# Optimization experiments

Measured on AMD Instinct MI355X. Metric: run time of the kernel, lower is better.

## Reference

```python
import jax, jax.numpy as jnp
import numpy as np

T, B, D = 256, 64, 512


def setup_inputs() -> dict:
    key = jax.random.key(0)
    ks = jax.random.split(key, 9)
    s = 1.0 / np.sqrt(D)  # torch Linear default init scale (uniform), use scaled normal
    return {
        "x": jax.random.normal(ks[0], (T, B, D), dtype=jnp.float32),
        "y": jax.random.normal(ks[1], (T, B, D), dtype=jnp.float32),
        "Wr": jax.random.normal(ks[2], (D, D), dtype=jnp.float32) * s,
        "Ur": jax.random.normal(ks[3], (D, D), dtype=jnp.float32) * s,
        "Wz": jax.random.normal(ks[4], (D, D), dtype=jnp.float32) * s,
        "Uz": jax.random.normal(ks[5], (D, D), dtype=jnp.float32) * s,
        "Wg": jax.random.normal(ks[6], (D, D), dtype=jnp.float32) * s,
        "Ug": jax.random.normal(ks[7], (D, D), dtype=jnp.float32) * s,
        "bg": jnp.full((D,), 2.0, dtype=jnp.float32),
    }


def reference(x, y, Wr, Ur, Wz, Uz, Wg, Ug, bg):
    # GTrXL gating unit. torch Linear(y) == y @ W.T
    r = jax.nn.sigmoid(jnp.einsum("tbd,ed->tbe", y, Wr) + jnp.einsum("tbd,ed->tbe", x, Ur))
    z = jax.nn.sigmoid(jnp.einsum("tbd,ed->tbe", y, Wz) + jnp.einsum("tbd,ed->tbe", x, Uz) - bg)
    h = jnp.tanh(jnp.einsum("tbd,ed->tbe", y, Wg) + jnp.einsum("tbd,ed->tbe", r * x, Ug))
    g = (1.0 - z) * x + z * h  # (T, B, D)
    return g
```

## Files before the change

### kernel.cpp

```cpp
#include <hip/hip_runtime.h>
#include <stdint.h>

typedef unsigned short u16;
typedef __attribute__((ext_vector_type(8))) __bf16 bf16x8;
typedef __attribute__((ext_vector_type(4))) float f32x4;

#define Dn 512
#define Mn 16384


__device__ __forceinline__ u16 f2bf(float f) {
  unsigned u = __float_as_uint(f);
  u += 0x7fffu + ((u >> 16) & 1u);
  return (u16)(u >> 16);
}

__device__ __forceinline__ float bf2f(u16 b) {
  return __uint_as_float(((unsigned)b) << 16);
}

__device__ __forceinline__ void async16(const u16* g, u16* l) {
  __builtin_amdgcn_global_load_lds(
      (const __attribute__((address_space(1))) unsigned int*)g,
      (__attribute__((address_space(3))) unsigned int*)l, 16, 0, 0);
}

__device__ __forceinline__ float sigmoidf_(float v) {
  return 1.f / (1.f + __expf(-v));
}

__global__ void cast_all(const float* __restrict__ y, const float* __restrict__ x,
                         const float* w0, const float* w1, const float* w2,
                         const float* w3, const float* w4, const float* w5,
                         u16* __restrict__ yb, u16* __restrict__ xb,
                         u16* __restrict__ wb) {
  int b = blockIdx.x;
  const float* src;
  u16* dst;
  if (b < 8192) {
    src = y; dst = yb;
  } else if (b < 16384) {
    src = x; dst = xb; b -= 8192;
  } else {
    b -= 16384;
    const int wi = b >> 8;
    b &= 255;
    src = wi == 0 ? w0 : wi == 1 ? w1 : wi == 2 ? w2 : wi == 3 ? w3 : wi == 4 ? w4 : w5;
    dst = wb + wi * 262144;
  }
  const int i4 = b * 256 + (int)threadIdx.x;
  float4 v = ((const float4*)src)[i4];
  ushort4 o;
  o.x = f2bf(v.x); o.y = f2bf(v.y); o.z = f2bf(v.z); o.w = f2bf(v.w);
  ((ushort4*)dst)[i4] = o;
}

__global__ __launch_bounds__(256, 2) void gemm_rz(
    const u16* __restrict__ yb, const u16* __restrict__ xb,
    const u16* __restrict__ wb,
    const float* __restrict__ bg,
    u16* __restrict__ rxb, u16* __restrict__ zb) {
  __shared__ u16 smem[24576];
  u16* sY = smem;
  u16* sX = smem + 4096;
  u16* sW = smem + 8192;

  const int tid = threadIdx.x;
  const int lane = tid & 63;
  const int wave = tid >> 6;
  const int waveM = wave >> 1, waveN = wave & 1;
  const int mb = blockIdx.x >> 2, nb = blockIdx.x & 3;
  const int rowStart = mb * 128, colStart = nb * 128;
  const int wbyte = (tid & 192) * 16;
  const int lm = lane & 15, quad = lane >> 4;

  const int srow = tid >> 2;
  const int scol = (((tid & 3) ^ ((tid >> 3) & 3)) * 8);

  const int aswz = (quad ^ ((lm >> 1) & 3)) * 8;

  f32x4 accR[4][4] = {};
  f32x4 accZ[4][4] = {};

  for (int k0 = 0; k0 < Dn; k0 += 32) {
#pragma unroll
    for (int s = 0; s < 2; ++s) {
      async16(yb + (size_t)(rowStart + s * 64 + srow) * Dn + k0 + scol,
              (u16*)((char*)sY + s * 4096 + wbyte));
      async16(xb + (size_t)(rowStart + s * 64 + srow) * Dn + k0 + scol,
              (u16*)((char*)sX + s * 4096 + wbyte));
    }
#pragma unroll
    for (int w = 0; w < 4; ++w)
#pragma unroll
      for (int s = 0; s < 2; ++s)
        async16(wb + (size_t)w * 262144 +
                    (size_t)(colStart + s * 64 + srow) * Dn + k0 + scol,
                (u16*)((char*)sW + w * 8192 + s * 4096 + wbyte));
    __syncthreads();

    bf16x8 ay[4], ax[4], bw[4];
#pragma unroll
    for (int i = 0; i < 4; ++i) {
      const int off = (waveM * 64 + i * 16 + lm) * 32 + aswz;
      ay[i] = *(const bf16x8*)(sY + off);
      ax[i] = *(const bf16x8*)(sX + off);
    }
#pragma unroll
    for (int j = 0; j < 4; ++j)
      bw[j] = *(const bf16x8*)(sW + 0 * 4096 + (waveN * 64 + j * 16 + lm) * 32 + aswz);
#pragma unroll
    for (int i = 0; i < 4; ++i)
#pragma unroll
      for (int j = 0; j < 4; ++j)
        accR[i][j] = __builtin_amdgcn_mfma_f32_16x16x32_bf16(ay[i], bw[j], accR[i][j], 0, 0, 0);
#pragma unroll
    for (int j = 0; j < 4; ++j)
      bw[j] = *(const bf16x8*)(sW + 1 * 4096 + (waveN * 64 + j * 16 + lm) * 32 + aswz);
#pragma unroll
    for (int i = 0; i < 4; ++i)
#pragma unroll
      for (int j = 0; j < 4; ++j)
        accR[i][j] = __builtin_amdgcn_mfma_f32_16x16x32_bf16(ax[i], bw[j], accR[i][j], 0, 0, 0);
#pragma unroll
    for (int j = 0; j < 4; ++j)
      bw[j] = *(const bf16x8*)(sW + 2 * 4096 + (waveN * 64 + j * 16 + lm) * 32 + aswz);
#pragma unroll
    for (int i = 0; i < 4; ++i)
#pragma unroll
      for (int j = 0; j < 4; ++j)
        accZ[i][j] = __builtin_amdgcn_mfma_f32_16x16x32_bf16(ay[i], bw[j], accZ[i][j], 0, 0, 0);
#pragma unroll
    for (int j = 0; j < 4; ++j)
      bw[j] = *(const bf16x8*)(sW + 3 * 4096 + (waveN * 64 + j * 16 + lm) * 32 + aswz);
#pragma unroll
    for (int i = 0; i < 4; ++i)
#pragma unroll
      for (int j = 0; j < 4; ++j)
        accZ[i][j] = __builtin_amdgcn_mfma_f32_16x16x32_bf16(ax[i], bw[j], accZ[i][j], 0, 0, 0);
    __syncthreads();
  }

#pragma unroll
  for (int j = 0; j < 4; ++j) {
    const int e = colStart + waveN * 64 + j * 16 + lm;
    const float bgv = bg[e];
#pragma unroll
    for (int i = 0; i < 4; ++i) {
      const int m0 = rowStart + waveM * 64 + i * 16 + quad * 4;
#pragma unroll
      for (int rg = 0; rg < 4; ++rg) {
        const size_t idx = (size_t)(m0 + rg) * Dn + e;
        const float r = sigmoidf_(accR[i][j][rg]);
        rxb[idx] = f2bf(r * bf2f(xb[idx]));
        zb[idx] = f2bf(sigmoidf_(accZ[i][j][rg] - bgv));
      }
    }
  }
}

__global__ __launch_bounds__(256, 2) void gemm_gu(
    const u16* __restrict__ yb, const u16* __restrict__ rxb,
    const u16* __restrict__ wg,
    const u16* __restrict__ zb, const u16* __restrict__ xb,
    float* __restrict__ out) {
  __shared__ u16 smem[16384];
  u16* sA = smem;
  u16* sB = smem + 8192;

  const int tid = threadIdx.x;
  const int lane = tid & 63;
  const int wave = tid >> 6;
  const int waveM = wave >> 1, waveN = wave & 1;
  const int mb = blockIdx.x >> 2, nb = blockIdx.x & 3;
  const int rowStart = mb * 128, colStart = nb * 128;
  const int wbyte = (tid & 192) * 16;
  const int lm = lane & 15, quad = lane >> 4;

  const int srow = tid >> 3;
  const int scol = (((tid & 7) ^ ((tid >> 3) & 7)) * 8);
  const int lswz = lm & 7;

  f32x4 acc[4][4] = {};

  for (int kq = 0; kq < 16; ++kq) {
    const int half = kq >> 3;
    const int k0 = (kq & 7) * 64;
    const u16* abase = half ? rxb : yb;
    const u16* wbase = wg + (size_t)half * 262144;
#pragma unroll
    for (int s = 0; s < 4; ++s) {
      async16(abase + (size_t)(rowStart + s * 32 + srow) * Dn + k0 + scol,
              (u16*)((char*)sA + s * 4096 + wbyte));
      async16(wbase + (size_t)(colStart + s * 32 + srow) * Dn + k0 + scol,
              (u16*)((char*)sB + s * 4096 + wbyte));
    }
    __syncthreads();

#pragma unroll
    for (int kk = 0; kk < 2; ++kk) {
      bf16x8 aa[4], bw[4];
#pragma unroll
      for (int i = 0; i < 4; ++i)
        aa[i] = *(const bf16x8*)(sA + (waveM * 64 + i * 16 + lm) * 64 +
                                 ((kk * 4 + quad) ^ lswz) * 8);
#pragma unroll
      for (int j = 0; j < 4; ++j)
        bw[j] = *(const bf16x8*)(sB + (waveN * 64 + j * 16 + lm) * 64 +
                                 ((kk * 4 + quad) ^ lswz) * 8);
#pragma unroll
      for (int i = 0; i < 4; ++i)
#pragma unroll
        for (int j = 0; j < 4; ++j)
          acc[i][j] = __builtin_amdgcn_mfma_f32_16x16x32_bf16(aa[i], bw[j], acc[i][j], 0, 0, 0);
    }
    __syncthreads();
  }

#pragma unroll
  for (int j = 0; j < 4; ++j) {
    const int e = colStart + waveN * 64 + j * 16 + lm;
#pragma unroll
    for (int i = 0; i < 4; ++i) {
      const int m0 = rowStart + waveM * 64 + i * 16 + quad * 4;
#pragma unroll
      for (int rg = 0; rg < 4; ++rg) {
        const size_t idx = (size_t)(m0 + rg) * Dn + e;
        const float pre = acc[i][j][rg];
        const float ex = __expf(-2.f * pre);
        const float h = (1.f - ex) / (1.f + ex);
        const float z = bf2f(zb[idx]);
        const float xv = bf2f(xb[idx]);
        out[idx] = (1.f - z) * xv + z * h;
      }
    }
  }
}

extern "C" void kernel_launch(void* const* d_in, const int* in_sizes, int n_in,
                              void* d_out, int out_size, void* d_ws, size_t ws_size,
                              hipStream_t stream) {
  const float* x  = (const float*)d_in[0];
  const float* y  = (const float*)d_in[1];
  const float* Wr = (const float*)d_in[2];
  const float* Ur = (const float*)d_in[3];
  const float* Wz = (const float*)d_in[4];
  const float* Uz = (const float*)d_in[5];
  const float* Wg = (const float*)d_in[6];
  const float* Ug = (const float*)d_in[7];
  const float* bg = (const float*)d_in[8];
  float* out = (float*)d_out;

  char* ws = (char*)d_ws;
  u16* yb  = (u16*)(ws);
  u16* xb  = (u16*)(ws + 16777216);
  u16* rxb = (u16*)(ws + 2 * 16777216);
  u16* wb  = (u16*)(ws + 3 * 16777216);
  u16* zb  = (u16*)(ws + 3 * 16777216 + 3145728);

  cast_all<<<17920, 256, 0, stream>>>(y, x, Wr, Ur, Wz, Uz, Wg, Ug, yb, xb, wb);
  gemm_rz<<<512, 256, 0, stream>>>(yb, xb, wb, bg, rxb, zb);
  gemm_gu<<<512, 256, 0, stream>>>(yb, rxb, wb + (size_t)4 * 262144, zb, xb, out);
}
```

Baseline: 214.7 us.

## Pack weights as concatenated K=1024 matrices and split r/z GEMM into separate tiles

The weight-cast kernel now writes Wr|Ur and Wz|Uz side by side into one [1024 x 1024] bf16 matrix, and Wg|Ug into a [512 x 1024] matrix. The r/z GEMM becomes a single K=1024 GEMM over [y|x] with N=1024, launched as 1024 blocks of 128x128 tiles, using the gu kernel's 64-wide K loop and swizzle. Each block holds one accumulator set instead of two, which lowers register pressure and allows launch_bounds of 4 blocks per CU. The trade-off is that the A tiles (y and x) are now loaded twice, once by the r-column blocks and once by the z-column blocks.

```diff
diff --git a/kernel.cpp b/kernel.cpp
--- a/kernel.cpp
+++ b/kernel.cpp
@@ -33,135 +33,130 @@
                          const float* w0, const float* w1, const float* w2,
                          const float* w3, const float* w4, const float* w5,
                          u16* __restrict__ yb, u16* __restrict__ xb,
-                         u16* __restrict__ wb) {
+                         u16* __restrict__ bRZ, u16* __restrict__ bG) {
   int b = blockIdx.x;
-  const float* src;
-  u16* dst;
-  if (b < 8192) {
-    src = y; dst = yb;
-  } else if (b < 16384) {
-    src = x; dst = xb; b -= 8192;
-  } else {
-    b -= 16384;
-    const int wi = b >> 8;
-    b &= 255;
-    src = wi == 0 ? w0 : wi == 1 ? w1 : wi == 2 ? w2 : wi == 3 ? w3 : wi == 4 ? w4 : w5;
-    dst = wb + wi * 262144;
-  }
-  const int i4 = b * 256 + (int)threadIdx.x;
+  const int t = (int)threadIdx.x;
+  if (b < 16384) {
+    const float* src;
+    u16* dst;
+    if (b < 8192) { src = y; dst = yb; }
+    else          { src = x; dst = xb; b -= 8192; }
+    const int i4 = b * 256 + t;
+    float4 v = ((const float4*)src)[i4];
+    ushort4 o;
+    o.x = f2bf(v.x); o.y = f2bf(v.y); o.z = f2bf(v.z); o.w = f2bf(v.w);
+    ((ushort4*)dst)[i4] = o;
+    return;
+  }
+  b -= 16384;
+  const int wi = b >> 8;
+  const int bb = b & 255;
+  const float* src = wi == 0 ? w0 : wi == 1 ? w1 : wi == 2 ? w2
+                   : wi == 3 ? w3 : wi == 4 ? w4 : w5;
+  const int i4 = bb * 256 + t;
+  const int e  = i4 >> 7;
+  const int c4 = i4 & 127;
   float4 v = ((const float4*)src)[i4];
   ushort4 o;
   o.x = f2bf(v.x); o.y = f2bf(v.y); o.z = f2bf(v.z); o.w = f2bf(v.w);
-  ((ushort4*)dst)[i4] = o;
-}
-
-__global__ __launch_bounds__(256, 2) void gemm_rz(
+  ushort4* base = (wi >= 4) ? (ushort4*)bG : (ushort4*)bRZ;
+  const int row = e + ((wi == 2 || wi == 3) ? 512 : 0);
+  const int off = row * 256 + c4 + ((wi & 1) ? 128 : 0);
+  base[off] = o;
+}
+
+__global__ __launch_bounds__(256, 4) void gemm_rz1(
     const u16* __restrict__ yb, const u16* __restrict__ xb,
-    const u16* __restrict__ wb,
-    const float* __restrict__ bg,
+    const u16* __restrict__ bRZ, const float* __restrict__ bg,
     u16* __restrict__ rxb, u16* __restrict__ zb) {
-  __shared__ u16 smem[24576];
-  u16* sY = smem;
-  u16* sX = smem + 4096;
-  u16* sW = smem + 8192;
+  __shared__ u16 smem[16384];
+  u16* sA = smem;
+  u16* sB = smem + 8192;
 
   const int tid = threadIdx.x;
   const int lane = tid & 63;
   const int wave = tid >> 6;
   const int waveM = wave >> 1, waveN = wave & 1;
-  const int mb = blockIdx.x >> 2, nb = blockIdx.x & 3;
+  const int nb = blockIdx.x & 7, mb = blockIdx.x >> 3;
   const int rowStart = mb * 128, colStart = nb * 128;
   const int wbyte = (tid & 192) * 16;
   const int lm = lane & 15, quad = lane >> 4;
 
-  const int srow = tid >> 2;
-  const int scol = (((tid & 3) ^ ((tid >> 3) & 3)) * 8);
-
-  const int aswz = (quad ^ ((lm >> 1) & 3)) * 8;
-
-  f32x4 accR[4][4] = {};
-  f32x4 accZ[4][4] = {};
-
-  for (int k0 = 0; k0 < Dn; k0 += 32) {
-#pragma unroll
-    for (int s = 0; s < 2; ++s) {
-      async16(yb + (size_t)(rowStart + s * 64 + srow) * Dn + k0 + scol,
-              (u16*)((char*)sY + s * 4096 + wbyte));
-      async16(xb + (size_t)(rowStart + s * 64 + srow) * Dn + k0 + scol,
-              (u16*)((char*)sX + s * 4096 + wbyte));
-    }
-#pragma unroll
-    for (int w = 0; w < 4; ++w)
-#pragma unroll
-      for (int s = 0; s < 2; ++s)
-        async16(wb + (size_t)w * 262144 +
-                    (size_t)(colStart + s * 64 + srow) * Dn + k0 + scol,
-                (u16*)((char*)sW + w * 8192 + s * 4096 + wbyte));
-    __syncthreads();
-
-    bf16x8 ay[4], ax[4], bw[4];
-#pragma unroll
-    for (int i = 0; i < 4; ++i) {
-      const int off = (waveM * 64 + i * 16 + lm) * 32 + aswz;
-      ay[i] = *(const bf16x8*)(sY + off);
-      ax[i] = *(const bf16x8*)(sX + off);
-    }
-#pragma unroll
-    for (int j = 0; j < 4; ++j)
-      bw[j] = *(const bf16x8*)(sW + 0 * 4096 + (waveN * 64 + j * 16 + lm) * 32 + aswz);
-#pragma unroll
-    for (int i = 0; i < 4; ++i)
+  const int srow = tid >> 3;
+  const int scol = (((tid & 7) ^ ((tid >> 3) & 7)) * 8);
+  const int lswz = lm & 7;
+
+  f32x4 acc[4][4] = {};
+
+  for (int kq = 0; kq < 16; ++kq) {
+    const int half = kq >> 3;
+    const int k0 = (kq & 7) * 64;
+    const u16* abase = half ? xb : yb;
+#pragma unroll
+    for (int s = 0; s < 4; ++s) {
+      async16(abase + (size_t)(rowStart + s * 32 + srow) * 512 + k0 + scol,
+              (u16*)((char*)sA + s * 4096 + wbyte));
+      async16(bRZ + (size_t)(colStart + s * 32 + srow) * 1024 + kq * 64 + scol,
+              (u16*)((char*)sB + s * 4096 + wbyte));
+    }
+    __syncthreads();
+
+#pragma unroll
+    for (int kk = 0; kk < 2; ++kk) {
+      bf16x8 aa[4], bw[4];
+#pragma unroll
+      for (int i = 0; i < 4; ++i)
+        aa[i] = *(const bf16x8*)(sA + (waveM * 64 + i * 16 + lm) * 64 +
+                                 ((kk * 4 + quad) ^ lswz) * 8);
 #pragma unroll
       for (int j = 0; j < 4; ++j)
-        accR[i][j] = __builtin_amdgcn_mfma_f32_16x16x32_bf16(ay[i], bw[j], accR[i][j], 0, 0, 0);
-#pragma unroll
-    for (int j = 0; j < 4; ++j)
-      bw[j] = *(const bf16x8*)(sW + 1 * 4096 + (waveN * 64 + j * 16 + lm) * 32 + aswz);
-#pragma unroll
-    for (int i = 0; i < 4; ++i)
-#pragma unroll
-      for (int j = 0; j < 4; ++j)
-        accR[i][j] = __builtin_amdgcn_mfma_f32_16x16x32_bf16(ax[i], bw[j], accR[i][j], 0, 0, 0);
-#pragma unroll
-    for (int j = 0; j < 4; ++j)
-      bw[j] = *(const bf16x8*)(sW + 2 * 4096 + (waveN * 64 + j * 16 + lm) * 32 + aswz);
-#pragma unroll
-    for (int i = 0; i < 4; ++i)
-#pragma unroll
-      for (int j = 0; j < 4; ++j)
-        accZ[i][j] = __builtin_amdgcn_mfma_f32_16x16x32_bf16(ay[i], bw[j], accZ[i][j], 0, 0, 0);
-#pragma unroll
-    for (int j = 0; j < 4; ++j)
-      bw[j] = *(const bf16x8*)(sW + 3 * 4096 + (waveN * 64 + j * 16 + lm) * 32 + aswz);
-#pragma unroll
-    for (int i = 0; i < 4; ++i)
-#pragma unroll
-      for (int j = 0; j < 4; ++j)
-        accZ[i][j] = __builtin_amdgcn_mfma_f32_16x16x32_bf16(ax[i], bw[j], accZ[i][j], 0, 0, 0);
-    __syncthreads();
-  }
-
-#pragma unroll
-  for (int j = 0; j < 4; ++j) {
-    const int e = colStart + waveN * 64 + j * 16 + lm;
-    const float bgv = bg[e];
-#pragma unroll
-    for (int i = 0; i < 4; ++i) {
-      const int m0 = rowStart + waveM * 64 + i * 16 + quad * 4;
-#pragma unroll
-      for (int rg = 0; rg < 4; ++rg) {
-        const size_t idx = (size_t)(m0 + rg) * Dn + e;
-        const float r = sigmoidf_(accR[i][j][rg]);
-        rxb[idx] = f2bf(r * bf2f(xb[idx]));
-        zb[idx] = f2bf(sigmoidf_(accZ[i][j][rg] - bgv));
+        bw[j] = *(const bf16x8*)(sB + (waveN * 64 + j * 16 + lm) * 64 +
+                                 ((kk * 4 + quad) ^ lswz) * 8);
+#pragma unroll
+      for (int i = 0; i < 4; ++i)
+#pragma unroll
+        for (int j = 0; j < 4; ++j)
+          acc[i][j] = __builtin_amdgcn_mfma_f32_16x16x32_bf16(aa[i], bw[j], acc[i][j], 0, 0, 0);
+    }
+    __syncthreads();
+  }
+
+  if (colStart < 512) {
+#pragma unroll
+    for (int j = 0; j < 4; ++j) {
+      const int e = colStart + waveN * 64 + j * 16 + lm;
+#pragma unroll
+      for (int i = 0; i < 4; ++i) {
+        const int m0 = rowStart + waveM * 64 + i * 16 + quad * 4;
+#pragma unroll
+        for (int rg = 0; rg < 4; ++rg) {
+          const size_t idx = (size_t)(m0 + rg) * 512 + e;
+          const float r = sigmoidf_(acc[i][j][rg]);
+          rxb[idx] = f2bf(r * bf2f(xb[idx]));
+        }
       }
     }
-  }
-}
-
-__global__ __launch_bounds__(256, 2) void gemm_gu(
+  } else {
+#pragma unroll
+    for (int j = 0; j < 4; ++j) {
+      const int e = colStart - 512 + waveN * 64 + j * 16 + lm;
+      const float bgv = bg[e];
+#pragma unroll
+      for (int i = 0; i < 4; ++i) {
+        const int m0 = rowStart + waveM * 64 + i * 16 + quad * 4;
+#pragma unroll
+        for (int rg = 0; rg < 4; ++rg) {
+          const size_t idx = (size_t)(m0 + rg) * 512 + e;
+          zb[idx] = f2bf(sigmoidf_(acc[i][j][rg] - bgv));
+        }
+      }
+    }
+  }
+}
+
+__global__ __launch_bounds__(256, 4) void gemm_gu1(
     const u16* __restrict__ yb, const u16* __restrict__ rxb,
-    const u16* __restrict__ wg,
+    const u16* __restrict__ bG,
     const u16* __restrict__ zb, const u16* __restrict__ xb,
     float* __restrict__ out) {
   __shared__ u16 smem[16384];
@@ -172,7 +167,7 @@
   const int lane = tid & 63;
   const int wave = tid >> 6;
   const int waveM = wave >> 1, waveN = wave & 1;
-  const int mb = blockIdx.x >> 2, nb = blockIdx.x & 3;
+  const int nb = blockIdx.x & 3, mb = blockIdx.x >> 2;
   const int rowStart = mb * 128, colStart = nb * 128;
   const int wbyte = (tid & 192) * 16;
   const int lm = lane & 15, quad = lane >> 4;
@@ -187,12 +182,11 @@
     const int half = kq >> 3;
     const int k0 = (kq & 7) * 64;
     const u16* abase = half ? rxb : yb;
-    const u16* wbase = wg + (size_t)half * 262144;
 #pragma unroll
     for (int s = 0; s < 4; ++s) {
-      async16(abase + (size_t)(rowStart + s * 32 + srow) * Dn + k0 + scol,
+      async16(abase + (size_t)(rowStart + s * 32 + srow) * 512 + k0 + scol,
               (u16*)((char*)sA + s * 4096 + wbyte));
-      async16(wbase + (size_t)(colStart + s * 32 + srow) * Dn + k0 + scol,
+      async16(bG + (size_t)(colStart + s * 32 + srow) * 1024 + kq * 64 + scol,
               (u16*)((char*)sB + s * 4096 + wbyte));
     }
     __syncthreads();
@@ -225,7 +219,7 @@
       const int m0 = rowStart + waveM * 64 + i * 16 + quad * 4;
 #pragma unroll
       for (int rg = 0; rg < 4; ++rg) {
-        const size_t idx = (size_t)(m0 + rg) * Dn + e;
+        const size_t idx = (size_t)(m0 + rg) * 512 + e;
         const float pre = acc[i][j][rg];
         const float ex = __expf(-2.f * pre);
         const float h = (1.f - ex) / (1.f + ex);
@@ -255,10 +249,11 @@
   u16* yb  = (u16*)(ws);
   u16* xb  = (u16*)(ws + 16777216);
   u16* rxb = (u16*)(ws + 2 * 16777216);
-  u16* wb  = (u16*)(ws + 3 * 16777216);
-  u16* zb  = (u16*)(ws + 3 * 16777216 + 3145728);
-
-  cast_all<<<17920, 256, 0, stream>>>(y, x, Wr, Ur, Wz, Uz, Wg, Ug, yb, xb, wb);
-  gemm_rz<<<512, 256, 0, stream>>>(yb, xb, wb, bg, rxb, zb);
-  gemm_gu<<<512, 256, 0, stream>>>(yb, rxb, wb + (size_t)4 * 262144, zb, xb, out);
-}
+  u16* zb  = (u16*)(ws + 3 * 16777216);
+  u16* bRZ = (u16*)(ws + 4 * 16777216);
+  u16* bG  = (u16*)(ws + 4 * 16777216 + 2097152);
+
+  cast_all<<<17920, 256, 0, stream>>>(y, x, Wr, Ur, Wz, Uz, Wg, Ug, yb, xb, bRZ, bG);
+  gemm_rz1<<<1024, 256, 0, stream>>>(yb, xb, bRZ, bg, rxb, zb);
+  gemm_gu1<<<512, 256, 0, stream>>>(yb, rxb, bG, zb, xb, out);
+}
```

After: 226.8 us. 1.06x slower.
